# Kernel optimization log

Hardware: AMD Instinct MI355X
Metric: run time of the kernel (lower is better)

The kernel has to match this reference:

```python
import jax, jax.numpy as jnp
import numpy as np

IGNORE_LABEL = -1.0
POS_THR, NEG_THR = 0.5, 0.4
BBOX_CLIP = float(np.log(1000.0 / 16.0))


def box_overlap(box, gt):
    # box [M,4], gt [G,4] -> IoU [M,G]  (legacy +1 box widths)
    area_b = (box[:, 2] - box[:, 0] + 1) * (box[:, 3] - box[:, 1] + 1)
    area_g = (gt[:, 2] - gt[:, 0] + 1) * (gt[:, 3] - gt[:, 1] + 1)
    iw = jnp.minimum(box[:, None, 2], gt[None, :, 2]) - jnp.maximum(box[:, None, 0], gt[None, :, 0]) + 1
    ih = jnp.minimum(box[:, None, 3], gt[None, :, 3]) - jnp.maximum(box[:, None, 1], gt[None, :, 1]) + 1
    inter = jnp.maximum(iw, 0.0) * jnp.maximum(ih, 0.0)
    union = area_b[:, None] + area_g[None, :] - inter
    return inter / jnp.maximum(union, 1.0)


def bbox_transform_inv(anchors, deltas):
    # decode deltas [M,4] against anchors [M,4]
    w = anchors[:, 2] - anchors[:, 0] + 1
    h = anchors[:, 3] - anchors[:, 1] + 1
    cx = anchors[:, 0] + 0.5 * w
    cy = anchors[:, 1] + 0.5 * h
    pcx = cx + deltas[:, 0] * w
    pcy = cy + deltas[:, 1] * h
    pw = w * jnp.exp(jnp.minimum(deltas[:, 2], BBOX_CLIP))
    ph = h * jnp.exp(jnp.minimum(deltas[:, 3], BBOX_CLIP))
    return jnp.stack([pcx - 0.5 * pw, pcy - 0.5 * ph, pcx + 0.5 * pw, pcy + 0.5 * ph], axis=1)


def bbox_transform(anchors, gt):
    # encode gt [M,4] against anchors [M,4]
    aw = anchors[:, 2] - anchors[:, 0] + 1
    ah = anchors[:, 3] - anchors[:, 1] + 1
    acx = anchors[:, 0] + 0.5 * aw
    acy = anchors[:, 1] + 0.5 * ah
    gw = gt[:, 2] - gt[:, 0] + 1
    gh = gt[:, 3] - gt[:, 1] + 1
    gcx = gt[:, 0] + 0.5 * gw
    gcy = gt[:, 1] + 0.5 * gh
    return jnp.stack([(gcx - acx) / aw, (gcy - acy) / ah, jnp.log(gw / aw), jnp.log(gh / ah)], axis=1)


def rpn_anchor_target(boxes, anchors4):
    # boxes [n,G,5] -> labels [n,A,2] (top-2 EMD matching), targets [n,2A,4]
    anc2 = jnp.repeat(anchors4, 2, axis=0)  # interleaved [a0,a0,a1,a1,...]
    def per_image(gt):
        ov = box_overlap(anchors4, gt[:, :4])                     # [A,G]
        valid = gt[:, 4] != IGNORE_LABEL
        ov = jnp.where(valid[None, :], ov, -1.0)
        vals, idx = jax.lax.top_k(ov, 2)                          # [A,2]
        labels = jnp.where(vals >= POS_THR, 1.0,
                           jnp.where(vals < NEG_THR, 0.0, IGNORE_LABEL))
        matched = gt[idx.reshape(-1), :4]                         # [2A,4]
        targets = bbox_transform(anc2, matched)
        return labels, targets
    return jax.vmap(per_image)(boxes)


def anchor_iou_target(boxes, anchors4, pred_reg):
    # decode both predictions per anchor, IoU vs gt, then best / 2nd-best match value
    A = anchors4.shape[0]
    anc2 = jnp.repeat(anchors4, 2, axis=0)
    def per_image(gt, off):
        off = off.reshape(-1, 4)                                  # [2A,4]
        dt = bbox_transform_inv(anc2, off)
        ov = box_overlap(dt, gt[:, :4])                           # [2A,G]
        keep = 1.0 - (gt[:, 4] == IGNORE_LABEL).astype(ov.dtype)
        ov = ov * keep[None, :]
        ov = ov.reshape(A, 2, -1)
        a, b = ov[:, 0, :], ov[:, 1, :]
        ia = jnp.argmax(a, axis=1)
        aval = jnp.take_along_axis(a, ia[:, None], axis=1)        # [A,1]
        b = b.at[jnp.arange(A), ia].set(0.0)                      # scatter best slot to 0
        ib = jnp.argmax(b, axis=1)
        bval = jnp.take_along_axis(b, ib[:, None], axis=1)
        return jnp.concatenate([aval, bval], axis=1)              # [A,2]
    return jax.vmap(per_image)(boxes, pred_reg)


def sigmoid_ce_retina(pred, label, alpha=0.25, gamma=2.0):
    # focal loss; pred [n,M,1] probs, label [n,M] in {-1,0,1}
    mask = (label != IGNORE_LABEL).astype(pred.dtype)
    vlabel = label * mask
    onehot = (vlabel == 1.0).astype(pred.dtype)[:, :, None]
    pos = (1.0 - pred) ** gamma * onehot * jnp.log(pred)
    neg = pred ** gamma * (1.0 - onehot) * jnp.log(1.0 - pred)
    loss = -(alpha * pos + (1.0 - alpha) * neg).sum(axis=2) * mask
    npos = jnp.maximum((label > 0).sum(), 1)
    return loss.sum() / npos


def fg_mask(label):
    # label not background(0) and not ignore(-1)
    return ((label != 0.0) & (label != IGNORE_LABEL)).astype(jnp.float32)


def smooth_l1_retina(pred, gt, label, sigma=3.0):
    s2 = sigma * sigma
    x = pred - gt
    ax = jnp.abs(x)
    val = jnp.where(ax < 1.0 / s2, 0.5 * s2 * x * x, ax - 0.5 / s2)
    mask = fg_mask(label)
    return (val.sum(axis=2) * mask).sum() / jnp.maximum(mask.sum(), 1.0)


def iou_l1(pred, target, label):
    mask = fg_mask(label)
    return (jnp.abs(pred - target) * mask).sum() / jnp.maximum(mask.sum(), 1.0)


def softmax_loss_fn(score, label):
    # score [M,c], label [M] ints with -1 = ignore
    logp = jax.nn.log_softmax(score, axis=1)
    mask = label != -1
    vlabel = jnp.where(mask, label, 0).astype(jnp.int32)
    picked = jnp.take_along_axis(logp, vlabel[:, None], axis=1)[:, 0]
    return -(picked * mask).sum() / jnp.maximum(mask.sum(), 1)


def setup_inputs() -> dict:
    key = jax.random.key(0)
    ks = jax.random.split(key, 10)
    n, A, G = 2, 120000, 300
    pred_cls = jax.nn.sigmoid(jax.random.normal(ks[0], (n, A, 2), jnp.float32))
    rpn_num_prob = jax.random.normal(ks[1], (n, A, 2), jnp.float32)
    pred_reg = 0.2 * jax.random.normal(ks[2], (n, A, 8), jnp.float32)
    rpn_iou = jax.nn.sigmoid(jax.random.normal(ks[3], (n, A, 2), jnp.float32))
    cx = jax.random.uniform(ks[4], (A,), minval=0.0, maxval=1024.0)
    cy = jax.random.uniform(ks[5], (A,), minval=0.0, maxval=1024.0)
    w = jax.random.uniform(ks[6], (A,), minval=16.0, maxval=256.0)
    h = jax.random.uniform(ks[7], (A,), minval=16.0, maxval=256.0)
    anchors = jnp.stack([cx - 0.5 * w, cy - 0.5 * h, cx + 0.5 * w, cy + 0.5 * h], axis=1)
    kx, ky, kw, kh, kl = jax.random.split(ks[8], 5)
    gx = jax.random.uniform(kx, (n, G), minval=0.0, maxval=900.0)
    gy = jax.random.uniform(ky, (n, G), minval=0.0, maxval=900.0)
    gw = jax.random.uniform(kw, (n, G), minval=20.0, maxval=200.0)
    gh = jax.random.uniform(kh, (n, G), minval=20.0, maxval=200.0)
    glab = jnp.where(jax.random.uniform(kl, (n, G)) < 0.95, 1.0, -1.0)
    boxes = jnp.stack([gx, gy, gx + gw, gy + gh, glab], axis=2)
    im_info = jnp.concatenate([
        jnp.tile(jnp.array([[1024.0, 1024.0, 1.0, 1024.0, 1024.0]], jnp.float32), (n, 1)),
        jnp.full((n, 1), float(G), jnp.float32)], axis=1)
    return {"pred_cls": pred_cls, "rpn_num_prob": rpn_num_prob, "pred_reg": pred_reg,
            "anchors": anchors, "rpn_iou": rpn_iou, "boxes": boxes, "im_info": im_info}


def reference(pred_cls, rpn_num_prob, pred_reg, anchors, rpn_iou, boxes, im_info):
    n = pred_cls.shape[0]
    anchors4 = anchors[:, :4]
    # anchor targets and iou targets are computed under no_grad in the original
    rpn_labels, rpn_target_boxes = jax.lax.stop_gradient(rpn_anchor_target(boxes, anchors4))
    ious_target = jax.lax.stop_gradient(anchor_iou_target(boxes, anchors4, pred_reg))
    target_boxes = rpn_target_boxes.reshape(n, -1, 4)   # [n,2A,4]
    cls_prob = pred_cls.reshape(n, -1, 1)               # [n,2A,1]
    offsets = pred_reg.reshape(n, -1, 4)                # [n,2A,4]
    a = rpn_labels[:, :, 0]
    b = rpn_labels[:, :, 1]
    ignores = b - (a == 0.0).astype(b.dtype) * (b != 0.0).astype(b.dtype)
    labels = jnp.stack([a, ignores], axis=2).reshape(n, -1)  # [n,2A]
    cls_loss = sigmoid_ce_retina(cls_prob, labels, 0.25, 2.0)
    bbox_loss = smooth_l1_retina(offsets, target_boxes, labels)
    lab2 = labels.reshape(n, -1, 2)
    iou_loss = iou_l1(rpn_iou, ious_target, lab2)
    nlabels = (lab2 > 0).sum(axis=2).reshape(-1).astype(jnp.int32) - 1  # in {-1,0,1}
    num_loss = softmax_loss_fn(rpn_num_prob.reshape(-1, rpn_num_prob.shape[2]), nlabels)
    # order: rpn_cls_loss, rpn_bbox_loss, rpn_iou_loss, rpn_num_loss
    return jnp.stack([cls_loss, 2.0 * bbox_loss, 2.0 * iou_loss, num_loss])
```

## Files before the change

kernel.cpp:

```cpp
#include <hip/hip_runtime.h>
#include <math.h>

#define G_MAX 512

#define XB 64
#define YB 16
#define NBINS 1024
#define SCLX (64.0f / 900.0f)
#define SCLY (16.0f / 900.0f)

__device__ __forceinline__ int xbin(float v) {
  int b = (int)(v * SCLX);
  return min(max(b, 0), XB - 1);
}
__device__ __forceinline__ int ybin(float v) {
  int b = (int)(v * SCLY);
  return min(max(b, 0), YB - 1);
}

__device__ __forceinline__ float waveSum(float v) {
#pragma unroll
  for (int o = 32; o > 0; o >>= 1) v += __shfl_down(v, o, 64);
  return v;
}

__device__ __forceinline__ float huber9(float x) {
  float ax = fabsf(x);
  return (ax < (1.0f / 9.0f)) ? 4.5f * x * x : ax - (0.5f / 9.0f);
}

__device__ __forceinline__ float iouExact(float bx0, float by0, float bx1, float by1,
                                          float areab, float4 g, float areag) {
  float gx1 = g.z - 1.0f, gy1 = g.w - 1.0f;
  float iw = fminf(bx1, gx1) - fmaxf(bx0, g.x) + 1.0f;
  float ih = fminf(by1, gy1) - fmaxf(by0, g.y) + 1.0f;
  float inter = fmaxf(iw, 0.f) * fmaxf(ih, 0.f);
  float uni = areab + areag - inter;
  return inter / fmaxf(uni, 1.0f);
}

__device__ __forceinline__ uint32_t packKey(float x0, float y0, float x1p, float y1p,
                                            float area, float4 gb, float ga,
                                            uint32_t g) {
  float iw = fminf(x1p, gb.z) - fmaxf(x0, gb.x);
  float ih = fminf(y1p, gb.w) - fmaxf(y0, gb.y);
  float inter = fmaxf(iw, 0.f) * ih;
  float key = (area + ga) * __builtin_amdgcn_rcpf(inter);
  return (__float_as_uint(key) & 0xFFFFFE00u) | g;
}

__global__ __launch_bounds__(256) void retina_main(
    const float* __restrict__ pred_cls,
    const float* __restrict__ rpn_num,
    const float* __restrict__ pred_reg,
    const float* __restrict__ anchors,
    const float* __restrict__ rpn_iou,
    const float* __restrict__ boxes,
    int A, int G,
    double* __restrict__ partial)
{
  __shared__ float4 sBox[G_MAX];
  __shared__ float2 sMeta[G_MAX];
  __shared__ unsigned short sO2S[G_MAX];
  __shared__ int sCnt[NBINS];
  __shared__ int sStart[NBINS + 1];
  __shared__ int sWsum[4];
  __shared__ float sWaveMax[4][2];
  __shared__ float sSpanX, sSpanY;
  __shared__ float sRed[4][7];
  __shared__ float sStash[128][10];
  __shared__ float2 sRes[128];
  __shared__ unsigned char sList[128];
  __shared__ int sNum;

  const int img = blockIdx.y;
  const int seg = threadIdx.x & 1;
  const int duo = threadIdx.x >> 1;
  const int i   = blockIdx.x * 128 + duo;
  const int ic  = (i < A) ? i : (A - 1);
  const float* gtb = boxes + (size_t)img * G * 5;

  float4 a4 = *(const float4*)(anchors + (size_t)ic * 4);
  float ax0 = a4.x, ay0 = a4.y, ax1 = a4.z, ay1 = a4.w;
  float aw = ax1 - ax0 + 1.0f, ah = ay1 - ay0 + 1.0f;
  float areaa = aw * ah;
  float acx = ax0 + 0.5f * aw, acy = ay0 + 0.5f * ah;
  float ax1p = ax1 + 1.0f, ay1p = ay1 + 1.0f;

  float d0 = 0.f, d1 = 0.f, d2 = 0.f, d3 = 0.f;
  float d4 = 0.f, d5 = 0.f, d6 = 0.f, d7 = 0.f;
  float pcv0 = 0.f, pcv1 = 0.f, riv0 = 0.f, riv1 = 0.f, sn0 = 0.f, sn1 = 0.f;
  if (seg == 0) {
    const float* dp = pred_reg + ((size_t)img * A + ic) * 8;
    d0 = dp[0]; d1 = dp[1]; d2 = dp[2]; d3 = dp[3];
    d4 = dp[4]; d5 = dp[5]; d6 = dp[6]; d7 = dp[7];
    const float* pc = pred_cls + ((size_t)img * A + ic) * 2;
    pcv0 = pc[0]; pcv1 = pc[1];
    const float* ri = rpn_iou + ((size_t)img * A + ic) * 2;
    riv0 = ri[0]; riv1 = ri[1];
    const float* sp = rpn_num + ((size_t)img * A + ic) * 2;
    sn0 = sp[0]; sn1 = sp[1];
  }

  if (threadIdx.x == 0) sNum = 0;
  for (int b = threadIdx.x; b < NBINS; b += 256) sCnt[b] = 0;
  for (int s = G + threadIdx.x; s < G_MAX; s += 256) {
    sBox[s] = make_float4(0.f, 0.f, 1.f, 1.f);
    sMeta[s] = make_float2(1e30f, __uint_as_float((unsigned)s));
    sO2S[s] = (unsigned short)G;
  }
  __syncthreads();

  float rx0[2], ry0[2], rx1[2], ry1[2], rlb[2];
  int ng = 0;
  for (int g = threadIdx.x; g < G; g += 256, ++ng) {
    rx0[ng] = gtb[g * 5 + 0]; ry0[ng] = gtb[g * 5 + 1];
    rx1[ng] = gtb[g * 5 + 2]; ry1[ng] = gtb[g * 5 + 3];
    rlb[ng] = gtb[g * 5 + 4];
    atomicAdd(&sCnt[(ybin(ry0[ng]) << 6) | xbin(rx0[ng])], 1);
  }
  __syncthreads();

  {
    int t = threadIdx.x;
    int b0 = sCnt[t * 4 + 0], b1 = sCnt[t * 4 + 1];
    int b2 = sCnt[t * 4 + 2], b3 = sCnt[t * 4 + 3];
    int tsum = b0 + b1 + b2 + b3;
    int lane = t & 63, wid = t >> 6;
    int incl = tsum;
#pragma unroll
    for (int o = 1; o < 64; o <<= 1) {
      int u = __shfl_up(incl, o, 64);
      if (lane >= o) incl += u;
    }
    if (lane == 63) sWsum[wid] = incl;
    __syncthreads();
    int woff = 0;
    for (int w = 0; w < wid; ++w) woff += sWsum[w];
    int excl = woff + incl - tsum;
    sStart[t * 4 + 0] = excl;
    sStart[t * 4 + 1] = excl + b0;
    sStart[t * 4 + 2] = excl + b0 + b1;
    sStart[t * 4 + 3] = excl + b0 + b1 + b2;
    if (t == 255) sStart[NBINS] = excl + tsum;
    sCnt[t * 4 + 0] = excl;
    sCnt[t * 4 + 1] = excl + b0;
    sCnt[t * 4 + 2] = excl + b0 + b1;
    sCnt[t * 4 + 3] = excl + b0 + b1 + b2;
  }
  __syncthreads();

  float mspanX = 0.f, mspanY = 0.f;
  {
    int g = threadIdx.x;
    for (int k = 0; k < ng; ++k, g += 256) {
      float x0 = rx0[k], y0 = ry0[k], x1 = rx1[k], y1 = ry1[k], lb = rlb[k];
      int pos = atomicAdd(&sCnt[(ybin(y0) << 6) | xbin(x0)], 1);
      float x1p = x1 + 1.0f, y1p = y1 + 1.0f;
      sBox[pos] = make_float4(x0, y0, x1p, y1p);
      sMeta[pos] = make_float2(
          (lb != -1.0f) ? (x1 - x0 + 1.0f) * (y1 - y0 + 1.0f) : 1e30f,
          __uint_as_float((unsigned)g));
      sO2S[g] = (unsigned short)pos;
      mspanX = fmaxf(mspanX, x1p - x0);
      mspanY = fmaxf(mspanY, y1p - y0);
    }
  }
#pragma unroll
  for (int m = 32; m > 0; m >>= 1) {
    mspanX = fmaxf(mspanX, __shfl_xor(mspanX, m, 64));
    mspanY = fmaxf(mspanY, __shfl_xor(mspanY, m, 64));
  }
  {
    int lane = threadIdx.x & 63, wid = threadIdx.x >> 6;
    if (lane == 0) { sWaveMax[wid][0] = mspanX; sWaveMax[wid][1] = mspanY; }
  }
  __syncthreads();
  if (threadIdx.x == 0) {
    sSpanX = fmaxf(fmaxf(sWaveMax[0][0], sWaveMax[1][0]),
                   fmaxf(sWaveMax[2][0], sWaveMax[3][0])) + 1.0f;
    sSpanY = fmaxf(fmaxf(sWaveMax[0][1], sWaveMax[1][1]),
                   fmaxf(sWaveMax[2][1], sWaveMax[3][1])) + 1.0f;
  }
  __syncthreads();
  const float spanX = sSpanX, spanY = sSpanY;

  float t_cls = 0.f, t_bbox = 0.f, t_iou = 0.f, t_num = 0.f;
  float t_npos = 0.f, t_nfg = 0.f, t_ncnt = 0.f;

  const float BBOX_CLIP = 4.1351666f;

  uint32_t an1 = 0xFFFFFFFFu, an2 = 0xFFFFFFFFu;
  {
    int xb0 = xbin(ax0 - spanX);
    int xb1 = xbin(ax1p);
    int yb0 = ybin(ay0 - spanY);
    int yb1 = ybin(ay1p);
    for (int yb = yb0; yb <= yb1; ++yb) {
      int lo = sStart[(yb << 6) + xb0];
      int hi = sStart[(yb << 6) + xb1 + 1];
#pragma unroll 2
      for (int s = lo + seg; s < hi; s += 2) {
        float4 gb = sBox[s];
        float2 mt = sMeta[s];
        uint32_t pk = packKey(ax0, ay0, ax1p, ay1p, areaa, gb, mt.x,
                              __float_as_uint(mt.y));
        uint32_t h = max(pk, an1);
        an1 = min(an1, pk);
        an2 = min(an2, h);
      }
    }
  }

  {
    uint32_t o1 = (uint32_t)__shfl_xor((int)an1, 1, 64);
    uint32_t o2 = (uint32_t)__shfl_xor((int)an2, 1, 64);
    uint32_t hi = max(an1, o1);
    an1 = min(an1, o1);
    an2 = min(min(an2, o2), hi);
  }

  bool fg0 = false, fg1 = false, needy = false;

  if (seg == 0 && i < A) {
    int og0 = (int)(an1 & 0x1FFu);
    int og1 = (int)(an2 & 0x1FFu);
    int s0 = sO2S[og0];
    int s1 = sO2S[og1];

    float4 g0 = sBox[s0]; float a0 = sMeta[s0].x; bool val0 = a0 < 1e29f;
    float v0 = val0 ? iouExact(ax0, ay0, ax1, ay1, areaa, g0, a0) : -1.0f;
    float4 g1 = sBox[s1]; float a1 = sMeta[s1].x; bool val1 = a1 < 1e29f;
    float v1 = val1 ? iouExact(ax0, ay0, ax1, ay1, areaa, g1, a1) : -1.0f;

    float la  = (v0 >= 0.5f) ? 1.0f : ((v0 < 0.4f) ? 0.0f : -1.0f);
    float lbv = (v1 >= 0.5f) ? 1.0f : ((v1 < 0.4f) ? 0.0f : -1.0f);
    float lab0 = la;
    float lab1 = lbv - (((la == 0.0f) && (lbv != 0.0f)) ? 1.0f : 0.0f);

    {
      float pv = pcv0;
      if (lab0 != -1.0f) {
        float l = (lab0 == 1.0f)
                      ? 0.25f * (1.0f - pv) * (1.0f - pv) * logf(pv)
                      : 0.75f * pv * pv * logf(1.0f - pv);
        t_cls -= l;
      }
      if (lab0 > 0.f) t_npos += 1.f;
      float qv = pcv1;
      if (lab1 != -1.0f) {
        float l = (lab1 == 1.0f)
                      ? 0.25f * (1.0f - qv) * (1.0f - qv) * logf(qv)
                      : 0.75f * qv * qv * logf(1.0f - qv);
        t_cls -= l;
      }
      if (lab1 > 0.f) t_npos += 1.f;
    }

    fg0 = (lab0 != 0.0f) && (lab0 != -1.0f);
    fg1 = (lab1 != 0.0f) && (lab1 != -1.0f);

    float raw = __builtin_amdgcn_rcpf(aw), rah = __builtin_amdgcn_rcpf(ah);

    if (fg0) {
      float mx1 = g0.z - 1.0f, my1 = g0.w - 1.0f;
      float gw = mx1 - g0.x + 1.0f, gh = my1 - g0.y + 1.0f;
      float gcx = g0.x + 0.5f * gw, gcy = g0.y + 0.5f * gh;
      float t0 = (gcx - acx) * raw, t1v = (gcy - acy) * rah;
      float t2 = logf(gw * raw), t3 = logf(gh * rah);
      t_bbox += huber9(d0 - t0) + huber9(d1 - t1v) + huber9(d2 - t2) + huber9(d3 - t3);
      t_nfg += 1.f;
    }
    if (fg1) {
      float mx1 = g1.z - 1.0f, my1 = g1.w - 1.0f;
      float gw = mx1 - g1.x + 1.0f, gh = my1 - g1.y + 1.0f;
      float gcx = g1.x + 0.5f * gw, gcy = g1.y + 0.5f * gh;
      float t0 = (gcx - acx) * raw, t1v = (gcy - acy) * rah;
      float t2 = logf(gw * raw), t3 = logf(gh * rah);
      t_bbox += huber9(d4 - t0) + huber9(d5 - t1v) + huber9(d6 - t2) + huber9(d7 - t3);
      t_nfg += 1.f;
    }

    {
      int nl = ((lab0 > 0.f) ? 1 : 0) + ((lab1 > 0.f) ? 1 : 0) - 1;
      if (nl != -1) {
        float m = fmaxf(sn0, sn1);
        float lse = m + logf(expf(sn0 - m) + expf(sn1 - m));
        float picked = ((nl == 0) ? sn0 : sn1) - lse;
        t_num -= picked;
        t_ncnt += 1.f;
      }
    }

    needy = fg0 || fg1;
    if (needy) {
      float p0cx = acx + d0 * aw, p0cy = acy + d1 * ah;
      float p0w = aw * expf(fminf(d2, BBOX_CLIP));
      float p0h = ah * expf(fminf(d3, BBOX_CLIP));
      float b0x0 = p0cx - 0.5f * p0w, b0y0 = p0cy - 0.5f * p0h;
      float b0x1 = p0cx + 0.5f * p0w, b0y1 = p0cy + 0.5f * p0h;
      float area0 = (b0x1 - b0x0 + 1.0f) * (b0y1 - b0y0 + 1.0f);

      float p1cx = acx + d4 * aw, p1cy = acy + d5 * ah;
      float p1w = aw * expf(fminf(d6, BBOX_CLIP));
      float p1h = ah * expf(fminf(d7, BBOX_CLIP));
      float b1x0 = p1cx - 0.5f * p1w, b1y0 = p1cy - 0.5f * p1h;
      float b1x1 = p1cx + 0.5f * p1w, b1y1 = p1cy + 0.5f * p1h;
      float area1 = (b1x1 - b1x0 + 1.0f) * (b1y1 - b1y0 + 1.0f);

      int slot = atomicAdd(&sNum, 1);
      sList[slot] = (unsigned char)duo;
      float* st = sStash[slot];
      st[0] = b0x0; st[1] = b0y0; st[2] = b0x1; st[3] = b0y1; st[4] = area0;
      st[5] = b1x0; st[6] = b1y0; st[7] = b1x1; st[8] = b1y1; st[9] = area1;
    }
  }
  __syncthreads();

  {
    int num = sNum;
    for (int sb = 0; sb < num; sb += 64) {
      int slot = sb + (threadIdx.x >> 2);
      int wseg = threadIdx.x & 3;
      if (slot < num) {
        const float* st = sStash[slot];
        float c0x0 = st[0], c0y0 = st[1], c0x1 = st[2], c0y1 = st[3], car0 = st[4];
        float c1x0 = st[5], c1y0 = st[6], c1x1 = st[7], c1y1 = st[8], car1 = st[9];
        float c0x1p = c0x1 + 1.0f, c0y1p = c0y1 + 1.0f;
        float c1x1p = c1x1 + 1.0f, c1y1p = c1y1 + 1.0f;

        uint32_t am = 0xFFFFFFFFu;
        uint32_t bk1 = 0xFFFFFFFFu, bk2 = 0xFFFFFFFFu;

        int xb0 = xbin(fminf(c0x0, c1x0) - spanX);
        int xb1 = xbin(fmaxf(c0x1p, c1x1p));
        int yb0 = ybin(fminf(c0y0, c1y0) - spanY);
        int yb1 = ybin(fmaxf(c0y1p, c1y1p));
        for (int yb = yb0; yb <= yb1; ++yb) {
          int lo = sStart[(yb << 6) + xb0];
          int hi = sStart[(yb << 6) + xb1 + 1];
#pragma unroll 2
          for (int s = lo + wseg; s < hi; s += 4) {
            float4 gb = sBox[s];
            float2 mt = sMeta[s];
            uint32_t og = __float_as_uint(mt.y);
            am = min(am, packKey(c0x0, c0y0, c0x1p, c0y1p, car0, gb, mt.x, og));
            uint32_t pk = packKey(c1x0, c1y0, c1x1p, c1y1p, car1, gb, mt.x, og);
            uint32_t hib = max(pk, bk1);
            bk1 = min(bk1, pk);
            bk2 = min(min(bk2, hib), bk2);
            bk2 = min(bk2, hib);
          }
        }

#pragma unroll
        for (int m = 1; m <= 2; m <<= 1) {
          am = min(am, (uint32_t)__shfl_xor((int)am, m, 64));
          uint32_t q1 = (uint32_t)__shfl_xor((int)bk1, m, 64);
          uint32_t q2 = (uint32_t)__shfl_xor((int)bk2, m, 64);
          uint32_t hib = max(bk1, q1);
          bk1 = min(bk1, q1);
          bk2 = min(min(bk2, q2), hib);
        }

        if (wseg == 0) {
          int ai  = (int)(am  & 0x1FFu);
          int bi  = (int)(bk1 & 0x1FFu);
          int bi2 = (int)(bk2 & 0x1FFu);
          int sa = sO2S[ai];
          float4 ga4 = sBox[sa]; float aav = sMeta[sa].x;
          float aval = (aav < 1e29f) ? iouExact(c0x0, c0y0, c0x1, c0y1, car0, ga4, aav) : 0.0f;
          int bIdx = (ai == bi) ? bi2 : bi;
          int sb2 = sO2S[bIdx];
          float4 gb4 = sBox[sb2]; float abv = sMeta[sb2].x;
          float bval = (abv < 1e29f) ? iouExact(c1x0, c1y0, c1x1, c1y1, car1, gb4, abv) : 0.0f;
          sRes[sList[slot]] = make_float2(aval, bval);
        }
      }
    }
  }
  __syncthreads();

  if (needy) {
    float2 r = sRes[duo];
    if (fg0) t_iou += fabsf(riv0 - r.x);
    if (fg1) t_iou += fabsf(riv1 - fmaxf(r.y, 0.0f));
  }

  float vals[7] = {t_cls, t_bbox, t_iou, t_num, t_npos, t_nfg, t_ncnt};
  int lane = threadIdx.x & 63;
  int wid = threadIdx.x >> 6;
#pragma unroll
  for (int k = 0; k < 7; ++k) {
    float s = waveSum(vals[k]);
    if (lane == 0) sRed[wid][k] = s;
  }
  __syncthreads();
  if (threadIdx.x < 7) {
    double s = (double)sRed[0][threadIdx.x] + (double)sRed[1][threadIdx.x] +
               (double)sRed[2][threadIdx.x] + (double)sRed[3][threadIdx.x];
    size_t bid = (size_t)blockIdx.y * gridDim.x + blockIdx.x;
    partial[bid * 8 + threadIdx.x] = s;
  }
}

__global__ __launch_bounds__(1024) void retina_finalize(
    const double* __restrict__ partial, int nB, float* __restrict__ out) {
  __shared__ double sRed[16][7];
  double loc[7] = {0.0, 0.0, 0.0, 0.0, 0.0, 0.0, 0.0};
  for (int b = threadIdx.x; b < nB; b += 1024) {
    const double* r = partial + (size_t)b * 8;
#pragma unroll
    for (int k = 0; k < 7; ++k) loc[k] += r[k];
  }
  int lane = threadIdx.x & 63;
  int wid = threadIdx.x >> 6;
#pragma unroll
  for (int k = 0; k < 7; ++k) {
    double v = loc[k];
#pragma unroll
    for (int o = 32; o > 0; o >>= 1) v += __shfl_down(v, o, 64);
    if (lane == 0) sRed[wid][k] = v;
  }
  __syncthreads();
  if (threadIdx.x == 0) {
    double t[7];
#pragma unroll
    for (int k = 0; k < 7; ++k) {
      double s = 0.0;
      for (int w = 0; w < 16; ++w) s += sRed[w][k];
      t[k] = s;
    }
    double dpos = t[4] > 1.0 ? t[4] : 1.0;
    double dfg  = t[5] > 1.0 ? t[5] : 1.0;
    double dcnt = t[6] > 1.0 ? t[6] : 1.0;
    out[0] = (float)(t[0] / dpos);
    out[1] = (float)(2.0 * t[1] / dfg);
    out[2] = (float)(2.0 * t[2] / dfg);
    out[3] = (float)(t[3] / dcnt);
  }
}

extern "C" void kernel_launch(void* const* d_in, const int* in_sizes, int n_in,
                              void* d_out, int out_size, void* d_ws, size_t ws_size,
                              hipStream_t stream) {
  const float* pred_cls = (const float*)d_in[0];
  const float* rpn_num  = (const float*)d_in[1];
  const float* pred_reg = (const float*)d_in[2];
  const float* anchors  = (const float*)d_in[3];
  const float* rpn_iou  = (const float*)d_in[4];
  const float* boxes    = (const float*)d_in[5];

  int A = in_sizes[3] / 4;
  int n = in_sizes[0] / (2 * A);
  int G = in_sizes[5] / (5 * n);

  double* partial = (double*)d_ws;

  int nBx = (A + 127) / 128;
  int nB = nBx * n;
  dim3 grid(nBx, n, 1);
  retina_main<<<grid, dim3(256, 1, 1), 0, stream>>>(
      pred_cls, rpn_num, pred_reg, anchors, rpn_iou, boxes, A, G, partial);
  retina_finalize<<<dim3(1, 1, 1), dim3(1024, 1, 1), 0, stream>>>(
      partial, nB, (float*)d_out);
}
```

Measured before the change: 130.5 us.

## Fold finalize into main kernel via last-block reduction and shrink spatial bins

Drops the separate finalize launch. Each block now bumps a global atomic counter after writing its partials, and the last block to finish reduces all partials and writes the losses, which removes a kernel launch and its gap. The x-bin grid is halved (32 by 16 bins) and the G_MAX box arrays are shrunk to cut shared memory, which may raise occupancy but makes each bin scan coarser. It also adds a memset launch, and G_MAX=384 assumes no more than 384 gt boxes.

```diff
diff --git a/kernel.cpp b/kernel.cpp
--- a/kernel.cpp
+++ b/kernel.cpp
@@ -1,12 +1,13 @@
 #include <hip/hip_runtime.h>
 #include <math.h>
 
-#define G_MAX 512
-
-#define XB 64
+#define G_MAX 384
+#define O2S_MAX 512
+
+#define XB 32
 #define YB 16
-#define NBINS 1024
-#define SCLX (64.0f / 900.0f)
+#define NBINS 512
+#define SCLX (32.0f / 900.0f)
 #define SCLY (16.0f / 900.0f)
 
 __device__ __forceinline__ int xbin(float v) {
@@ -56,22 +57,26 @@
     const float* __restrict__ anchors,
     const float* __restrict__ rpn_iou,
     const float* __restrict__ boxes,
-    int A, int G,
-    double* __restrict__ partial)
+    int A, int G, int totalBlocks, int nB,
+    double* __restrict__ partial,
+    unsigned int* __restrict__ cnt,
+    float* __restrict__ out)
 {
   __shared__ float4 sBox[G_MAX];
   __shared__ float2 sMeta[G_MAX];
-  __shared__ unsigned short sO2S[G_MAX];
+  __shared__ unsigned short sO2S[O2S_MAX];
   __shared__ int sCnt[NBINS];
   __shared__ int sStart[NBINS + 1];
   __shared__ int sWsum[4];
   __shared__ float sWaveMax[4][2];
   __shared__ float sSpanX, sSpanY;
   __shared__ float sRed[4][7];
+  __shared__ double sRedD[4][7];
   __shared__ float sStash[128][10];
   __shared__ float2 sRes[128];
   __shared__ unsigned char sList[128];
   __shared__ int sNum;
+  __shared__ int sLast;
 
   const int img = blockIdx.y;
   const int seg = threadIdx.x & 1;
@@ -107,8 +112,9 @@
   for (int s = G + threadIdx.x; s < G_MAX; s += 256) {
     sBox[s] = make_float4(0.f, 0.f, 1.f, 1.f);
     sMeta[s] = make_float2(1e30f, __uint_as_float((unsigned)s));
+  }
+  for (int s = G + threadIdx.x; s < O2S_MAX; s += 256)
     sO2S[s] = (unsigned short)G;
-  }
   __syncthreads();
 
   float rx0[2], ry0[2], rx1[2], ry1[2], rlb[2];
@@ -117,15 +123,14 @@
     rx0[ng] = gtb[g * 5 + 0]; ry0[ng] = gtb[g * 5 + 1];
     rx1[ng] = gtb[g * 5 + 2]; ry1[ng] = gtb[g * 5 + 3];
     rlb[ng] = gtb[g * 5 + 4];
-    atomicAdd(&sCnt[(ybin(ry0[ng]) << 6) | xbin(rx0[ng])], 1);
+    atomicAdd(&sCnt[(ybin(ry0[ng]) << 5) | xbin(rx0[ng])], 1);
   }
   __syncthreads();
 
   {
     int t = threadIdx.x;
-    int b0 = sCnt[t * 4 + 0], b1 = sCnt[t * 4 + 1];
-    int b2 = sCnt[t * 4 + 2], b3 = sCnt[t * 4 + 3];
-    int tsum = b0 + b1 + b2 + b3;
+    int b0 = sCnt[t * 2 + 0], b1 = sCnt[t * 2 + 1];
+    int tsum = b0 + b1;
     int lane = t & 63, wid = t >> 6;
     int incl = tsum;
 #pragma unroll
@@ -138,15 +143,11 @@
     int woff = 0;
     for (int w = 0; w < wid; ++w) woff += sWsum[w];
     int excl = woff + incl - tsum;
-    sStart[t * 4 + 0] = excl;
-    sStart[t * 4 + 1] = excl + b0;
-    sStart[t * 4 + 2] = excl + b0 + b1;
-    sStart[t * 4 + 3] = excl + b0 + b1 + b2;
+    sStart[t * 2 + 0] = excl;
+    sStart[t * 2 + 1] = excl + b0;
     if (t == 255) sStart[NBINS] = excl + tsum;
-    sCnt[t * 4 + 0] = excl;
-    sCnt[t * 4 + 1] = excl + b0;
-    sCnt[t * 4 + 2] = excl + b0 + b1;
-    sCnt[t * 4 + 3] = excl + b0 + b1 + b2;
+    sCnt[t * 2 + 0] = excl;
+    sCnt[t * 2 + 1] = excl + b0;
   }
   __syncthreads();
 
@@ -155,7 +156,7 @@
     int g = threadIdx.x;
     for (int k = 0; k < ng; ++k, g += 256) {
       float x0 = rx0[k], y0 = ry0[k], x1 = rx1[k], y1 = ry1[k], lb = rlb[k];
-      int pos = atomicAdd(&sCnt[(ybin(y0) << 6) | xbin(x0)], 1);
+      int pos = atomicAdd(&sCnt[(ybin(y0) << 5) | xbin(x0)], 1);
       float x1p = x1 + 1.0f, y1p = y1 + 1.0f;
       sBox[pos] = make_float4(x0, y0, x1p, y1p);
       sMeta[pos] = make_float2(
@@ -197,8 +198,8 @@
     int yb0 = ybin(ay0 - spanY);
     int yb1 = ybin(ay1p);
     for (int yb = yb0; yb <= yb1; ++yb) {
-      int lo = sStart[(yb << 6) + xb0];
-      int hi = sStart[(yb << 6) + xb1 + 1];
+      int lo = sStart[(yb << 5) + xb0];
+      int hi = sStart[(yb << 5) + xb1 + 1];
 #pragma unroll 2
       for (int s = lo + seg; s < hi; s += 2) {
         float4 gb = sBox[s];
@@ -337,8 +338,8 @@
         int yb0 = ybin(fminf(c0y0, c1y0) - spanY);
         int yb1 = ybin(fmaxf(c0y1p, c1y1p));
         for (int yb = yb0; yb <= yb1; ++yb) {
-          int lo = sStart[(yb << 6) + xb0];
-          int hi = sStart[(yb << 6) + xb1 + 1];
+          int lo = sStart[(yb << 5) + xb0];
+          int hi = sStart[(yb << 5) + xb1 + 1];
 #pragma unroll 2
           for (int s = lo + wseg; s < hi; s += 4) {
             float4 gb = sBox[s];
@@ -348,7 +349,6 @@
             uint32_t pk = packKey(c1x0, c1y0, c1x1p, c1y1p, car1, gb, mt.x, og);
             uint32_t hib = max(pk, bk1);
             bk1 = min(bk1, pk);
-            bk2 = min(min(bk2, hib), bk2);
             bk2 = min(bk2, hib);
           }
         }
@@ -396,48 +396,49 @@
     if (lane == 0) sRed[wid][k] = s;
   }
   __syncthreads();
+  size_t bid = (size_t)blockIdx.y * gridDim.x + blockIdx.x;
   if (threadIdx.x < 7) {
     double s = (double)sRed[0][threadIdx.x] + (double)sRed[1][threadIdx.x] +
                (double)sRed[2][threadIdx.x] + (double)sRed[3][threadIdx.x];
-    size_t bid = (size_t)blockIdx.y * gridDim.x + blockIdx.x;
     partial[bid * 8 + threadIdx.x] = s;
   }
-}
-
-__global__ __launch_bounds__(1024) void retina_finalize(
-    const double* __restrict__ partial, int nB, float* __restrict__ out) {
-  __shared__ double sRed[16][7];
-  double loc[7] = {0.0, 0.0, 0.0, 0.0, 0.0, 0.0, 0.0};
-  for (int b = threadIdx.x; b < nB; b += 1024) {
-    const double* r = partial + (size_t)b * 8;
-#pragma unroll
-    for (int k = 0; k < 7; ++k) loc[k] += r[k];
-  }
-  int lane = threadIdx.x & 63;
-  int wid = threadIdx.x >> 6;
-#pragma unroll
-  for (int k = 0; k < 7; ++k) {
-    double v = loc[k];
-#pragma unroll
-    for (int o = 32; o > 0; o >>= 1) v += __shfl_down(v, o, 64);
-    if (lane == 0) sRed[wid][k] = v;
-  }
+  __threadfence();
   __syncthreads();
   if (threadIdx.x == 0) {
-    double t[7];
+    unsigned int old = atomicAdd(cnt, 1u);
+    sLast = (old == (unsigned int)(totalBlocks - 1)) ? 1 : 0;
+  }
+  __syncthreads();
+
+  if (sLast) {
+    __threadfence();
+    double loc[7] = {0.0, 0.0, 0.0, 0.0, 0.0, 0.0, 0.0};
+    for (int b = threadIdx.x; b < nB; b += 256) {
+      double* r = partial + (size_t)b * 8;
+#pragma unroll
+      for (int k = 0; k < 7; ++k) loc[k] += atomicAdd(&r[k], 0.0);
+    }
 #pragma unroll
     for (int k = 0; k < 7; ++k) {
-      double s = 0.0;
-      for (int w = 0; w < 16; ++w) s += sRed[w][k];
-      t[k] = s;
-    }
-    double dpos = t[4] > 1.0 ? t[4] : 1.0;
-    double dfg  = t[5] > 1.0 ? t[5] : 1.0;
-    double dcnt = t[6] > 1.0 ? t[6] : 1.0;
-    out[0] = (float)(t[0] / dpos);
-    out[1] = (float)(2.0 * t[1] / dfg);
-    out[2] = (float)(2.0 * t[2] / dfg);
-    out[3] = (float)(t[3] / dcnt);
+      double v = loc[k];
+#pragma unroll
+      for (int o = 32; o > 0; o >>= 1) v += __shfl_down(v, o, 64);
+      if (lane == 0) sRedD[wid][k] = v;
+    }
+    __syncthreads();
+    if (threadIdx.x == 0) {
+      double t[7];
+#pragma unroll
+      for (int k = 0; k < 7; ++k)
+        t[k] = sRedD[0][k] + sRedD[1][k] + sRedD[2][k] + sRedD[3][k];
+      double dpos = t[4] > 1.0 ? t[4] : 1.0;
+      double dfg  = t[5] > 1.0 ? t[5] : 1.0;
+      double dcnt = t[6] > 1.0 ? t[6] : 1.0;
+      out[0] = (float)(t[0] / dpos);
+      out[1] = (float)(2.0 * t[1] / dfg);
+      out[2] = (float)(2.0 * t[2] / dfg);
+      out[3] = (float)(t[3] / dcnt);
+    }
   }
 }
 
@@ -455,13 +456,16 @@
   int n = in_sizes[0] / (2 * A);
   int G = in_sizes[5] / (5 * n);
 
-  double* partial = (double*)d_ws;
-
   int nBx = (A + 127) / 128;
   int nB = nBx * n;
+
+  double* partial = (double*)d_ws;
+  unsigned int* cnt = (unsigned int*)((char*)d_ws + (size_t)nB * 8 * sizeof(double));
+
+  hipMemsetAsync(cnt, 0, sizeof(unsigned int), stream);
+
   dim3 grid(nBx, n, 1);
   retina_main<<<grid, dim3(256, 1, 1), 0, stream>>>(
-      pred_cls, rpn_num, pred_reg, anchors, rpn_iou, boxes, A, G, partial);
-  retina_finalize<<<dim3(1, 1, 1), dim3(1024, 1, 1), 0, stream>>>(
-      partial, nB, (float*)d_out);
-}
+      pred_cls, rpn_num, pred_reg, anchors, rpn_iou, boxes,
+      A, G, nB, nB, partial, cnt, (float*)d_out);
+}
```

Result: slower. 230.3 us (+76.4%).
